# Performance work log

Hardware: AMD Instinct MI355X
Metric: run time of the kernel (lower is better)

Reference implementation:

```python
import jax, jax.numpy as jnp
import numpy as np

B, T, C = 2, 2048, 1024
H = 16
D = C // H  # head size 64


def setup_inputs() -> dict:
    key = jax.random.key(0)
    ks = jax.random.split(key, 9)
    s = 0.02
    return {
        "x": jax.random.normal(ks[0], (B, T, C), dtype=jnp.float32),
        "Wq": jax.random.normal(ks[1], (C, C), dtype=jnp.float32) * s,
        "bq": jnp.zeros((C,), dtype=jnp.float32),
        "Wk": jax.random.normal(ks[2], (C, C), dtype=jnp.float32) * s,
        "bk": jnp.zeros((C,), dtype=jnp.float32),
        "Wv": jax.random.normal(ks[3], (C, C), dtype=jnp.float32) * s,
        "bv": jnp.zeros((C,), dtype=jnp.float32),
        "Wo": jax.random.normal(ks[4], (C, C), dtype=jnp.float32) * s,
        "bo": jnp.zeros((C,), dtype=jnp.float32),
    }


def reference(x, Wq, bq, Wk, bk, Wv, bv, Wo, bo):
    b, t, c = x.shape
    scale = 1.0 / jnp.sqrt(jnp.asarray(D, dtype=x.dtype))
    # projections (torch Linear: x @ W.T + b), then split heads -> [B,H,T,D]
    def split_heads(y):
        return y.reshape(b, t, H, D).transpose(0, 2, 1, 3)
    q = split_heads(x @ Wq.T + bq)
    k = split_heads(x @ Wk.T + bk)
    v = split_heads(x @ Wv.T + bv)
    # scores [B,H,T,T], causal mask (triu above diagonal = -inf)
    attn = jnp.einsum("bhqd,bhkd->bhqk", q, k) * scale
    causal = jnp.tril(jnp.ones((t, t), dtype=bool))  # True = keep
    attn = jnp.where(causal[None, None], attn, -jnp.inf)
    attn = jax.nn.softmax(attn, axis=-1)
    # dropout p=0.0 -> identity
    y = jnp.einsum("bhqk,bhkd->bhqd", attn, v)
    y = y.transpose(0, 2, 1, 3).reshape(b, t, c)
    return y @ Wo.T + bo
```

## Files before the change

### kernel.cpp

```cpp
#include <hip/hip_runtime.h>
#include <hip/hip_bf16.h>
#include <stdint.h>
#include <stddef.h>


typedef __bf16 bf16;
typedef __attribute__((ext_vector_type(8))) __bf16 bf16x8;
typedef __attribute__((ext_vector_type(4))) __bf16 bf16x4;
typedef __attribute__((ext_vector_type(4))) float floatx4;

#define MFMA_16x16x32(A, B, C) __builtin_amdgcn_mfma_f32_16x16x32_bf16(A, B, C, 0, 0, 0)

static constexpr int T_SEQ = 2048;
static constexpr int CDIM  = 1024;

__device__ __forceinline__ void gl2lds16(const bf16* g, bf16* l) {
  __builtin_amdgcn_global_load_lds(
      (const __attribute__((address_space(1))) uint32_t*)g,
      (__attribute__((address_space(3))) uint32_t*)l, 16, 0, 0);
}

__global__ __launch_bounds__(256) void convert_kernel(
    const float* __restrict__ x, const float* __restrict__ Wq,
    const float* __restrict__ Wk, const float* __restrict__ Wv,
    const float* __restrict__ Wo,
    bf16* __restrict__ Xb, bf16* __restrict__ Wqkvb, bf16* __restrict__ Wob) {
  size_t i = ((size_t)blockIdx.x * 256 + threadIdx.x) * 4;
  const float* src;
  bf16* dst;
  size_t off;
  if (i < 4194304) {
    src = x; dst = Xb; off = i;
  } else {
    size_t r = i - 4194304;
    int wsel = (int)(r >> 20);
    off = r & 1048575;
    src = (wsel == 0) ? Wq : (wsel == 1) ? Wk : (wsel == 2) ? Wv : Wo;
    dst = (wsel < 3) ? (Wqkvb + ((size_t)wsel << 20)) : Wob;
  }
  float4 v = *(const float4*)(src + off);
  bf16x4 o;
  o[0] = (bf16)v.x; o[1] = (bf16)v.y; o[2] = (bf16)v.z; o[3] = (bf16)v.w;
  *(bf16x4*)(dst + off) = o;
}

__device__ __forceinline__ void gemm_tile_128x128(
    const bf16* __restrict__ A, const bf16* __restrict__ B, int K,
    bf16* As, bf16* Bs, floatx4 (&acc)[4][4], int bM, int bN) {
  const int tid = threadIdx.x;
  const int w = tid >> 6, l = tid & 63;
  const int wm = w & 1, wn = w >> 1;
  const int lr = l >> 3, cl = l & 7;
  const int fr = l & 15, q4 = l >> 4;

#pragma unroll
  for (int mi = 0; mi < 4; ++mi)
#pragma unroll
    for (int ni = 0; ni < 4; ++ni)
#pragma unroll
      for (int r = 0; r < 4; ++r) acc[mi][ni][r] = 0.0f;

  for (int k0 = 0; k0 < K; k0 += 64) {
#pragma unroll
    for (int i = 0; i < 4; ++i) {
      int row = i * 32 + w * 8 + lr;
      int cg = cl ^ (row & 7);
      gl2lds16(A + (size_t)(bM * 128 + row) * K + k0 + cg * 8,
               As + row * 64 + cl * 8);
      gl2lds16(B + (size_t)(bN * 128 + row) * K + k0 + cg * 8,
               Bs + row * 64 + cl * 8);
    }
    __syncthreads();
#pragma unroll
    for (int kk = 0; kk < 2; ++kk) {
      const int cgk = kk * 4 + q4;
      bf16x8 af[4], bfr[4];
#pragma unroll
      for (int mi = 0; mi < 4; ++mi) {
        int row = wm * 64 + mi * 16 + fr;
        af[mi] = *(const bf16x8*)(As + row * 64 + (cgk ^ (row & 7)) * 8);
      }
#pragma unroll
      for (int ni = 0; ni < 4; ++ni) {
        int row = wn * 64 + ni * 16 + fr;
        bfr[ni] = *(const bf16x8*)(Bs + row * 64 + (cgk ^ (row & 7)) * 8);
      }
#pragma unroll
      for (int mi = 0; mi < 4; ++mi)
#pragma unroll
        for (int ni = 0; ni < 4; ++ni)
          acc[mi][ni] = MFMA_16x16x32(af[mi], bfr[ni], acc[mi][ni]);
    }
    __syncthreads();
  }
}

__global__ __launch_bounds__(256) void gemm_qkv(
    const bf16* __restrict__ Xb, const bf16* __restrict__ Wqkvb,
    const float* __restrict__ bq, const float* __restrict__ bk,
    const float* __restrict__ bv,
    bf16* __restrict__ Qb, bf16* __restrict__ Kb, bf16* __restrict__ Vtb) {
  __shared__ __align__(16) bf16 smem[17408];
  bf16* As = smem;
  bf16* Bs = smem + 8192;
  bf16* Cs = smem;
  floatx4 acc[4][4];
  const int bM = blockIdx.x & 31;
  const int bN = blockIdx.x >> 5;
  gemm_tile_128x128(Xb, Wqkvb, CDIM, As, Bs, acc, bM, bN);

  const int tid = threadIdx.x;
  const int w = tid >> 6, l = tid & 63;
  const int wm = w & 1, wn = w >> 1;
  const int fc = l & 15, q4 = l >> 4;
  const int seg = bN >> 3;
  const float QSCALE = 0.125f * 1.44269504089f;
  const float* bp = (seg == 0) ? bq : (seg == 1) ? bk : bv;

#pragma unroll
  for (int ni = 0; ni < 4; ++ni) {
    int jl = wn * 64 + ni * 16 + fc;
    float bias = bp[(bN * 128 + jl) & 1023];
#pragma unroll
    for (int mi = 0; mi < 4; ++mi)
#pragma unroll
      for (int r = 0; r < 4; ++r) {
        int ttl = wm * 64 + mi * 16 + q4 * 4 + r;
        float val = acc[mi][ni][r] + bias;
        if (seg == 0) val *= QSCALE;
        int addr = (seg == 2) ? jl * 136 + ttl : ttl * 136 + jl;
        Cs[addr] = (bf16)val;
      }
  }
  __syncthreads();

  const int chunk = tid & 15;
  const int rb = (tid >> 4) * 8;
  if (seg < 2) {
    bf16* basep = (seg == 0) ? Qb : Kb;
#pragma unroll
    for (int u = 0; u < 8; ++u) {
      int maj = rb + u;
      bf16x8 vdat = *(const bf16x8*)(Cs + maj * 136 + chunk * 8);
      int n = bM * 128 + maj;
      int b = n >> 11, tt = n & 2047;
      int j = bN * 128 + chunk * 8;
      int h = (j >> 6) & 15, d = j & 63;
      *(bf16x8*)(basep + (((size_t)(b * 16 + h) * T_SEQ + tt) << 6) + d) = vdat;
    }
  } else {
#pragma unroll
    for (int u = 0; u < 8; ++u) {
      int maj = rb + u;
      bf16x8 vdat = *(const bf16x8*)(Cs + maj * 136 + chunk * 8);
      int j = bN * 128 + maj;
      int h = (j >> 6) & 15, d = j & 63;
      int n0 = bM * 128 + chunk * 8;
      int b = n0 >> 11, tt0 = n0 & 2047;
      *(bf16x8*)(Vtb + ((size_t)(b * 16 + h) * 64 + d) * T_SEQ + tt0) = vdat;
    }
  }
}

__global__ __launch_bounds__(256) void flash_attn(
    const bf16* __restrict__ Qb, const bf16* __restrict__ Kb,
    const bf16* __restrict__ Vtb, bf16* __restrict__ Ao) {
  __shared__ __align__(16) bf16 Ks[64 * 64];
  __shared__ __align__(16) bf16 Vs[64 * 64];
  __shared__ __align__(16) bf16 Ps[4][2][16 * 72];

  const int bh = blockIdx.x;
  const int qt2 = blockIdx.y;
  const int b = bh >> 4, h = bh & 15;
  const int tid = threadIdx.x;
  const int w = tid >> 6, l = tid & 63;
  const int fc = l & 15, q4 = l >> 4;
  const int lr = l >> 3, cl = l & 7;

  const bf16* Qg = Qb + (size_t)bh * T_SEQ * 64;
  const bf16* Kg = Kb + (size_t)bh * T_SEQ * 64;
  const bf16* Vg = Vtb + (size_t)bh * 64 * T_SEQ;
  const int qbase = qt2 * 128;

  bf16x8 qf[2][2];
#pragma unroll
  for (int mi = 0; mi < 2; ++mi) {
    const bf16* qrow = Qg + (size_t)(qbase + mi * 64 + w * 16 + fc) * 64;
#pragma unroll
    for (int kk = 0; kk < 2; ++kk)
      qf[mi][kk] = *(const bf16x8*)(qrow + kk * 32 + q4 * 8);
  }

  bf16x8 ones;
#pragma unroll
  for (int i = 0; i < 8; ++i) ones[i] = (bf16)1.0f;

  floatx4 o[2][4];
  floatx4 lacc[2];
#pragma unroll
  for (int mi = 0; mi < 2; ++mi) {
#pragma unroll
    for (int ds = 0; ds < 4; ++ds)
#pragma unroll
      for (int r = 0; r < 4; ++r) o[mi][ds][r] = 0.0f;
#pragma unroll
    for (int r = 0; r < 4; ++r) lacc[mi][r] = 0.0f;
  }

  const int kvmax = 2 * qt2 + 1;
  for (int kv = 0; kv <= kvmax; ++kv) {
    const int kvbase = kv * 64;
#pragma unroll
    for (int i = 0; i < 2; ++i) {
      int row = i * 32 + w * 8 + lr;
      int cg = cl ^ (row & 7);
      gl2lds16(Kg + (size_t)(kvbase + row) * 64 + cg * 8, Ks + row * 64 + cl * 8);
      gl2lds16(Vg + (size_t)row * T_SEQ + kvbase + cg * 8, Vs + row * 64 + cl * 8);
    }
    __syncthreads();

    const bool skip0 = (kv == 2 * qt2 + 1);

    floatx4 s[2][4];
#pragma unroll
    for (int mi = 0; mi < 2; ++mi)
#pragma unroll
      for (int ni = 0; ni < 4; ++ni)
#pragma unroll
        for (int r = 0; r < 4; ++r) s[mi][ni][r] = 0.0f;
#pragma unroll
    for (int kk = 0; kk < 2; ++kk) {
      const int cgk = kk * 4 + q4;
#pragma unroll
      for (int ni = 0; ni < 4; ++ni) {
        int row = ni * 16 + fc;
        bf16x8 kf = *(const bf16x8*)(Ks + row * 64 + (cgk ^ (row & 7)) * 8);
        if (!skip0) s[0][ni] = MFMA_16x16x32(qf[0][kk], kf, s[0][ni]);
        s[1][ni] = MFMA_16x16x32(qf[1][kk], kf, s[1][ni]);
      }
    }

#pragma unroll
    for (int mi = 0; mi < 2; ++mi) {
      if (mi == 0 && skip0) continue;
      const bool diag = (kv == 2 * qt2 + mi);
      if (diag) {
        int qc = w * 16 + q4 * 4;
#pragma unroll
        for (int ni = 0; ni < 4; ++ni)
#pragma unroll
          for (int r = 0; r < 4; ++r) {
            int kc = ni * 16 + fc;
            float p = (kc > qc + r) ? 0.0f : __builtin_amdgcn_exp2f(s[mi][ni][r]);
            Ps[w][mi][(q4 * 4 + r) * 72 + ni * 16 + fc] = (bf16)p;
          }
      } else {
#pragma unroll
        for (int ni = 0; ni < 4; ++ni)
#pragma unroll
          for (int r = 0; r < 4; ++r)
            Ps[w][mi][(q4 * 4 + r) * 72 + ni * 16 + fc] =
                (bf16)__builtin_amdgcn_exp2f(s[mi][ni][r]);
      }
    }

#pragma unroll
    for (int kk = 0; kk < 2; ++kk) {
      const int cgk = kk * 4 + q4;
      bf16x8 pf0, pf1;
      if (!skip0) pf0 = *(const bf16x8*)(&Ps[w][0][fc * 72 + kk * 32 + q4 * 8]);
      pf1 = *(const bf16x8*)(&Ps[w][1][fc * 72 + kk * 32 + q4 * 8]);
#pragma unroll
      for (int ds = 0; ds < 4; ++ds) {
        int row = ds * 16 + fc;
        bf16x8 vf = *(const bf16x8*)(Vs + row * 64 + (cgk ^ (row & 7)) * 8);
        if (!skip0) o[0][ds] = MFMA_16x16x32(pf0, vf, o[0][ds]);
        o[1][ds] = MFMA_16x16x32(pf1, vf, o[1][ds]);
      }
      if (!skip0) lacc[0] = MFMA_16x16x32(pf0, ones, lacc[0]);
      lacc[1] = MFMA_16x16x32(pf1, ones, lacc[1]);
    }
    __syncthreads();
  }

#pragma unroll
  for (int mi = 0; mi < 2; ++mi) {
    float inv[4];
#pragma unroll
    for (int r = 0; r < 4; ++r) inv[r] = __builtin_amdgcn_rcpf(lacc[mi][r]);
#pragma unroll
    for (int ds = 0; ds < 4; ++ds)
#pragma unroll
      for (int r = 0; r < 4; ++r) {
        int tt = qbase + mi * 64 + w * 16 + q4 * 4 + r;
        int col = h * 64 + ds * 16 + fc;
        Ao[((size_t)(b * T_SEQ + tt) << 10) + col] = (bf16)(o[mi][ds][r] * inv[r]);
      }
  }
}

__global__ __launch_bounds__(256) void gemm_out(
    const bf16* __restrict__ Ab, const bf16* __restrict__ Wob,
    const float* __restrict__ bo, float* __restrict__ Y) {
  __shared__ __align__(16) bf16 As[64 * 64];
  __shared__ __align__(16) bf16 Bs[128 * 64];
  const int bM = blockIdx.x & 63;
  const int bN = blockIdx.x >> 6;
  const int tid = threadIdx.x;
  const int w = tid >> 6, l = tid & 63;
  const int wm = w & 1, wn = w >> 1;
  const int lr = l >> 3, cl = l & 7;
  const int fr = l & 15, q4 = l >> 4;
  const int fc = fr;

  floatx4 acc[2][4];
#pragma unroll
  for (int mi = 0; mi < 2; ++mi)
#pragma unroll
    for (int ni = 0; ni < 4; ++ni)
#pragma unroll
      for (int r = 0; r < 4; ++r) acc[mi][ni][r] = 0.0f;

  for (int k0 = 0; k0 < CDIM; k0 += 64) {
#pragma unroll
    for (int i = 0; i < 2; ++i) {
      int row = i * 32 + w * 8 + lr;
      int cg = cl ^ (row & 7);
      gl2lds16(Ab + (size_t)(bM * 64 + row) * CDIM + k0 + cg * 8,
               As + row * 64 + cl * 8);
    }
#pragma unroll
    for (int i = 0; i < 4; ++i) {
      int row = i * 32 + w * 8 + lr;
      int cg = cl ^ (row & 7);
      gl2lds16(Wob + (size_t)(bN * 128 + row) * CDIM + k0 + cg * 8,
               Bs + row * 64 + cl * 8);
    }
    __syncthreads();
#pragma unroll
    for (int kk = 0; kk < 2; ++kk) {
      const int cgk = kk * 4 + q4;
      bf16x8 af[2], bfr[4];
#pragma unroll
      for (int mi = 0; mi < 2; ++mi) {
        int row = wm * 32 + mi * 16 + fr;
        af[mi] = *(const bf16x8*)(As + row * 64 + (cgk ^ (row & 7)) * 8);
      }
#pragma unroll
      for (int ni = 0; ni < 4; ++ni) {
        int row = wn * 64 + ni * 16 + fr;
        bfr[ni] = *(const bf16x8*)(Bs + row * 64 + (cgk ^ (row & 7)) * 8);
      }
#pragma unroll
      for (int mi = 0; mi < 2; ++mi)
#pragma unroll
        for (int ni = 0; ni < 4; ++ni)
          acc[mi][ni] = MFMA_16x16x32(af[mi], bfr[ni], acc[mi][ni]);
    }
    __syncthreads();
  }

#pragma unroll
  for (int ni = 0; ni < 4; ++ni) {
    int j = bN * 128 + wn * 64 + ni * 16 + fc;
    float bias = bo[j];
#pragma unroll
    for (int mi = 0; mi < 2; ++mi)
#pragma unroll
      for (int r = 0; r < 4; ++r) {
        int n = bM * 64 + wm * 32 + mi * 16 + q4 * 4 + r;
        Y[(size_t)n * CDIM + j] = acc[mi][ni][r] + bias;
      }
  }
}

extern "C" void kernel_launch(void* const* d_in, const int* in_sizes, int n_in,
                              void* d_out, int out_size, void* d_ws, size_t ws_size,
                              hipStream_t stream) {
  const float* x  = (const float*)d_in[0];
  const float* Wq = (const float*)d_in[1];
  const float* bq = (const float*)d_in[2];
  const float* Wk = (const float*)d_in[3];
  const float* bk = (const float*)d_in[4];
  const float* Wv = (const float*)d_in[5];
  const float* bv = (const float*)d_in[6];
  const float* Wo = (const float*)d_in[7];
  const float* bo = (const float*)d_in[8];
  float* Y = (float*)d_out;

  char* ws = (char*)d_ws;
  const size_t MB = 1024 * 1024;
  bf16* Xb    = (bf16*)(ws + 0);
  bf16* Wqkvb = (bf16*)(ws + 8 * MB);
  bf16* Wob   = (bf16*)(ws + 14 * MB);
  bf16* Qb    = (bf16*)(ws + 16 * MB);
  bf16* Kb    = (bf16*)(ws + 24 * MB);
  bf16* Vtb   = (bf16*)(ws + 32 * MB);
  bf16* Ao    = Xb;

  convert_kernel<<<8192, 256, 0, stream>>>(x, Wq, Wk, Wv, Wo, Xb, Wqkvb, Wob);
  gemm_qkv<<<32 * 24, 256, 0, stream>>>(Xb, Wqkvb, bq, bk, bv, Qb, Kb, Vtb);
  flash_attn<<<dim3(32, 16), 256, 0, stream>>>(Qb, Kb, Vtb, Ao);
  gemm_out<<<64 * 8, 256, 0, stream>>>(Ao, Wob, bo, Y);
}
```

Before: 208.4 us.

## Shrink flash-attention query tile to 64 rows and launch longest tiles first

```diff
diff --git a/kernel.cpp b/kernel.cpp
--- a/kernel.cpp
+++ b/kernel.cpp
@@ -167,10 +167,10 @@
     const bf16* __restrict__ Vtb, bf16* __restrict__ Ao) {
   __shared__ __align__(16) bf16 Ks[64 * 64];
   __shared__ __align__(16) bf16 Vs[64 * 64];
-  __shared__ __align__(16) bf16 Ps[4][2][16 * 72];
+  __shared__ __align__(16) bf16 Ps[4][16 * 72];
 
   const int bh = blockIdx.x;
-  const int qt2 = blockIdx.y;
+  const int qt = 31 - blockIdx.y;
   const int b = bh >> 4, h = bh & 15;
   const int tid = threadIdx.x;
   const int w = tid >> 6, l = tid & 63;
@@ -180,35 +180,26 @@
   const bf16* Qg = Qb + (size_t)bh * T_SEQ * 64;
   const bf16* Kg = Kb + (size_t)bh * T_SEQ * 64;
   const bf16* Vg = Vtb + (size_t)bh * 64 * T_SEQ;
-  const int qbase = qt2 * 128;
-
-  bf16x8 qf[2][2];
-#pragma unroll
-  for (int mi = 0; mi < 2; ++mi) {
-    const bf16* qrow = Qg + (size_t)(qbase + mi * 64 + w * 16 + fc) * 64;
-#pragma unroll
-    for (int kk = 0; kk < 2; ++kk)
-      qf[mi][kk] = *(const bf16x8*)(qrow + kk * 32 + q4 * 8);
-  }
+
+  const int qrow = qt * 64 + w * 16 + fc;
+  bf16x8 qf[2];
+  qf[0] = *(const bf16x8*)(Qg + (size_t)qrow * 64 + q4 * 8);
+  qf[1] = *(const bf16x8*)(Qg + (size_t)qrow * 64 + 32 + q4 * 8);
 
   bf16x8 ones;
 #pragma unroll
   for (int i = 0; i < 8; ++i) ones[i] = (bf16)1.0f;
 
-  floatx4 o[2][4];
-  floatx4 lacc[2];
-#pragma unroll
-  for (int mi = 0; mi < 2; ++mi) {
-#pragma unroll
-    for (int ds = 0; ds < 4; ++ds)
-#pragma unroll
-      for (int r = 0; r < 4; ++r) o[mi][ds][r] = 0.0f;
-#pragma unroll
-    for (int r = 0; r < 4; ++r) lacc[mi][r] = 0.0f;
-  }
-
-  const int kvmax = 2 * qt2 + 1;
-  for (int kv = 0; kv <= kvmax; ++kv) {
+  floatx4 o[4];
+  floatx4 lacc;
+#pragma unroll
+  for (int ds = 0; ds < 4; ++ds)
+#pragma unroll
+    for (int r = 0; r < 4; ++r) o[ds][r] = 0.0f;
+#pragma unroll
+  for (int r = 0; r < 4; ++r) lacc[r] = 0.0f;
+
+  for (int kv = 0; kv <= qt; ++kv) {
     const int kvbase = kv * 64;
 #pragma unroll
     for (int i = 0; i < 2; ++i) {
@@ -219,15 +210,11 @@
     }
     __syncthreads();
 
-    const bool skip0 = (kv == 2 * qt2 + 1);
-
-    floatx4 s[2][4];
-#pragma unroll
-    for (int mi = 0; mi < 2; ++mi)
-#pragma unroll
-      for (int ni = 0; ni < 4; ++ni)
-#pragma unroll
-        for (int r = 0; r < 4; ++r) s[mi][ni][r] = 0.0f;
+    floatx4 s[4];
+#pragma unroll
+    for (int ni = 0; ni < 4; ++ni)
+#pragma unroll
+      for (int r = 0; r < 4; ++r) s[ni][r] = 0.0f;
 #pragma unroll
     for (int kk = 0; kk < 2; ++kk) {
       const int cgk = kk * 4 + q4;
@@ -235,68 +222,55 @@
       for (int ni = 0; ni < 4; ++ni) {
         int row = ni * 16 + fc;
         bf16x8 kf = *(const bf16x8*)(Ks + row * 64 + (cgk ^ (row & 7)) * 8);
-        if (!skip0) s[0][ni] = MFMA_16x16x32(qf[0][kk], kf, s[0][ni]);
-        s[1][ni] = MFMA_16x16x32(qf[1][kk], kf, s[1][ni]);
-      }
-    }
-
-#pragma unroll
-    for (int mi = 0; mi < 2; ++mi) {
-      if (mi == 0 && skip0) continue;
-      const bool diag = (kv == 2 * qt2 + mi);
-      if (diag) {
-        int qc = w * 16 + q4 * 4;
-#pragma unroll
-        for (int ni = 0; ni < 4; ++ni)
-#pragma unroll
-          for (int r = 0; r < 4; ++r) {
-            int kc = ni * 16 + fc;
-            float p = (kc > qc + r) ? 0.0f : __builtin_amdgcn_exp2f(s[mi][ni][r]);
-            Ps[w][mi][(q4 * 4 + r) * 72 + ni * 16 + fc] = (bf16)p;
-          }
-      } else {
-#pragma unroll
-        for (int ni = 0; ni < 4; ++ni)
-#pragma unroll
-          for (int r = 0; r < 4; ++r)
-            Ps[w][mi][(q4 * 4 + r) * 72 + ni * 16 + fc] =
-                (bf16)__builtin_amdgcn_exp2f(s[mi][ni][r]);
-      }
+        s[ni] = MFMA_16x16x32(qf[kk], kf, s[ni]);
+      }
+    }
+
+    if (kv == qt) {
+      int qc = w * 16 + q4 * 4;
+#pragma unroll
+      for (int ni = 0; ni < 4; ++ni)
+#pragma unroll
+        for (int r = 0; r < 4; ++r) {
+          int kc = ni * 16 + fc;
+          float p = (kc > qc + r) ? 0.0f : __builtin_amdgcn_exp2f(s[ni][r]);
+          Ps[w][(q4 * 4 + r) * 72 + ni * 16 + fc] = (bf16)p;
+        }
+    } else {
+#pragma unroll
+      for (int ni = 0; ni < 4; ++ni)
+#pragma unroll
+        for (int r = 0; r < 4; ++r)
+          Ps[w][(q4 * 4 + r) * 72 + ni * 16 + fc] =
+              (bf16)__builtin_amdgcn_exp2f(s[ni][r]);
     }
 
 #pragma unroll
     for (int kk = 0; kk < 2; ++kk) {
+      bf16x8 pf = *(const bf16x8*)(&Ps[w][fc * 72 + kk * 32 + q4 * 8]);
       const int cgk = kk * 4 + q4;
-      bf16x8 pf0, pf1;
-      if (!skip0) pf0 = *(const bf16x8*)(&Ps[w][0][fc * 72 + kk * 32 + q4 * 8]);
-      pf1 = *(const bf16x8*)(&Ps[w][1][fc * 72 + kk * 32 + q4 * 8]);
 #pragma unroll
       for (int ds = 0; ds < 4; ++ds) {
         int row = ds * 16 + fc;
         bf16x8 vf = *(const bf16x8*)(Vs + row * 64 + (cgk ^ (row & 7)) * 8);
-        if (!skip0) o[0][ds] = MFMA_16x16x32(pf0, vf, o[0][ds]);
-        o[1][ds] = MFMA_16x16x32(pf1, vf, o[1][ds]);
-      }
-      if (!skip0) lacc[0] = MFMA_16x16x32(pf0, ones, lacc[0]);
-      lacc[1] = MFMA_16x16x32(pf1, ones, lacc[1]);
-    }
-    __syncthreads();
-  }
-
-#pragma unroll
-  for (int mi = 0; mi < 2; ++mi) {
-    float inv[4];
-#pragma unroll
-    for (int r = 0; r < 4; ++r) inv[r] = __builtin_amdgcn_rcpf(lacc[mi][r]);
-#pragma unroll
-    for (int ds = 0; ds < 4; ++ds)
-#pragma unroll
-      for (int r = 0; r < 4; ++r) {
-        int tt = qbase + mi * 64 + w * 16 + q4 * 4 + r;
-        int col = h * 64 + ds * 16 + fc;
-        Ao[((size_t)(b * T_SEQ + tt) << 10) + col] = (bf16)(o[mi][ds][r] * inv[r]);
-      }
-  }
+        o[ds] = MFMA_16x16x32(pf, vf, o[ds]);
+      }
+      lacc = MFMA_16x16x32(pf, ones, lacc);
+    }
+    __syncthreads();
+  }
+
+  float inv[4];
+#pragma unroll
+  for (int r = 0; r < 4; ++r) inv[r] = __builtin_amdgcn_rcpf(lacc[r]);
+#pragma unroll
+  for (int ds = 0; ds < 4; ++ds)
+#pragma unroll
+    for (int r = 0; r < 4; ++r) {
+      int tt = qt * 64 + w * 16 + q4 * 4 + r;
+      int col = h * 64 + ds * 16 + fc;
+      Ao[((size_t)(b * T_SEQ + tt) << 10) + col] = (bf16)(o[ds][r] * inv[r]);
+    }
 }
 
 __global__ __launch_bounds__(256) void gemm_out(
@@ -400,6 +374,6 @@
 
   convert_kernel<<<8192, 256, 0, stream>>>(x, Wq, Wk, Wv, Wo, Xb, Wqkvb, Wob);
   gemm_qkv<<<32 * 24, 256, 0, stream>>>(Xb, Wqkvb, bq, bk, bv, Qb, Kb, Vtb);
-  flash_attn<<<dim3(32, 16), 256, 0, stream>>>(Qb, Kb, Vtb, Ao);
+  flash_attn<<<dim3(32, 32), 256, 0, stream>>>(Qb, Kb, Vtb, Ao);
   gemm_out<<<64 * 8, 256, 0, stream>>>(Ao, Wob, bo, Y);
 }
```

After: 189.2 us. 9.2% less time.
